# Optimization experiments

Hardware: AMD Instinct MI355X
Metric: run time of the kernel (lower is better)

Reference implementation:

```python
import jax, jax.numpy as jnp
import numpy as np
from jax import lax

H = 1024
NH = 16
R = 32
B, S = 32, 1024
LN_EPS = 1e-5

def _gelu(x):
    return jax.nn.gelu(x, approximate=False)

def setup_inputs() -> dict:
    key = jax.random.key(0)
    ks = jax.random.split(key, 24)
    w = lambda k, shape: jax.random.normal(k, shape, jnp.float32) * 0.02
    d = {}
    d['computation_results'] = jax.random.normal(ks[0], (B, S, H), jnp.float32)
    d['max_steps'] = 16
    # rule selector: Linear(H,H), GELU, Linear(H,R)
    d['rule_w1'] = w(ks[1], (H, H)); d['rule_b1'] = jnp.zeros((H,))
    d['rule_w2'] = w(ks[2], (R, H)); d['rule_b2'] = jnp.zeros((R,))
    d['rule_emb'] = jax.random.normal(ks[3], (R, H), jnp.float32)
    # MultiheadAttention packed in-proj [3H,H] and out-proj [H,H]
    d['attn_in_w'] = w(ks[4], (3 * H, H)); d['attn_in_b'] = jnp.zeros((3 * H,))
    d['attn_out_w'] = w(ks[5], (H, H)); d['attn_out_b'] = jnp.zeros((H,))
    # 2-layer LSTM, PyTorch gate order i,f,g,o
    d['lstm_wih0'] = w(ks[6], (4 * H, H)); d['lstm_whh0'] = w(ks[7], (4 * H, H))
    d['lstm_bih0'] = jnp.zeros((4 * H,)); d['lstm_bhh0'] = jnp.zeros((4 * H,))
    d['lstm_wih1'] = w(ks[8], (4 * H, H)); d['lstm_whh1'] = w(ks[9], (4 * H, H))
    d['lstm_bih1'] = jnp.zeros((4 * H,)); d['lstm_bhh1'] = jnp.zeros((4 * H,))
    # step generator: Linear(H,2H), LayerNorm(2H), GELU, Linear(2H,H)
    d['gen_w1'] = w(ks[10], (2 * H, H)); d['gen_b1'] = jnp.zeros((2 * H,))
    d['gen_ln_g'] = jnp.ones((2 * H,)); d['gen_ln_b'] = jnp.zeros((2 * H,))
    d['gen_w2'] = w(ks[11], (H, 2 * H)); d['gen_b2'] = jnp.zeros((H,))
    # step validator: Linear(2H,H), GELU, Linear(H,1), Sigmoid
    d['val_w1'] = w(ks[12], (H, 2 * H)); d['val_b1'] = jnp.zeros((H,))
    d['val_w2'] = w(ks[13], (1, H)); d['val_b2'] = jnp.zeros((1,))
    # proof verifier: Linear(H,H), GELU, Linear(H,1), Sigmoid
    d['ver_w1'] = w(ks[14], (H, H)); d['ver_b1'] = jnp.zeros((H,))
    d['ver_w2'] = w(ks[15], (1, H)); d['ver_b2'] = jnp.zeros((1,))
    return d


def reference(computation_results, max_steps, rule_w1, rule_b1, rule_w2, rule_b2, rule_emb,
              attn_in_w, attn_in_b, attn_out_w, attn_out_b,
              lstm_wih0, lstm_whh0, lstm_bih0, lstm_bhh0,
              lstm_wih1, lstm_whh1, lstm_bih1, lstm_bhh1,
              gen_w1, gen_b1, gen_ln_g, gen_ln_b, gen_w2, gen_b2,
              val_w1, val_b1, val_w2, val_b2,
              ver_w1, ver_b1, ver_w2, ver_b2):
    comp = computation_results
    b, s, h = comp.shape
    dh = h // NH
    scale = dh ** -0.5
    wq, wk, wv = jnp.split(attn_in_w, 3, axis=0)
    bq, bk, bv = jnp.split(attn_in_b, 3, axis=0)
    # K/V projections of the static context, computed once outside the step loop
    K = (comp @ wk.T + bk).reshape(b, s, NH, dh)  # [B,S,NH,dh]
    V = (comp @ wv.T + bv).reshape(b, s, NH, dh)
    lstm_params = ((lstm_wih0, lstm_whh0, lstm_bih0, lstm_bhh0),
                   (lstm_wih1, lstm_whh1, lstm_bih1, lstm_bhh1))

    def step(carry, _):
        ps, hmem, cmem = carry  # ps: [B,H]; hmem/cmem: [2,B,H]
        # rule selection
        logits = _gelu(ps @ rule_w1.T + rule_b1) @ rule_w2.T + rule_b2
        probs = jax.nn.softmax(logits, axis=-1)  # [B,R]
        sel = probs @ rule_emb  # [B,H]
        # single-query multi-head attention over computation context
        q = (ps @ wq.T + bq).reshape(b, NH, dh) * scale
        scores = jnp.einsum('bhd,bshd->bhs', q, K)
        a = jax.nn.softmax(scores, axis=-1)  # [B,NH,S]
        ctx = jnp.einsum('bhs,bshd->bhd', a, V).reshape(b, h) @ attn_out_w.T + attn_out_b
        attn_avg = a.mean(axis=1)  # head-averaged weights, [B,S]
        # 2-layer LSTM cell, one timestep
        x = ps
        hs, cs = [], []
        for l, (wih, whh, bih, bhh) in enumerate(lstm_params):
            g = x @ wih.T + bih + hmem[l] @ whh.T + bhh
            gi, gf, gg, go = jnp.split(g, 4, axis=-1)
            cn = jax.nn.sigmoid(gf) * cmem[l] + jax.nn.sigmoid(gi) * jnp.tanh(gg)
            hn = jax.nn.sigmoid(go) * jnp.tanh(cn)
            hs.append(hn); cs.append(cn); x = hn
        mem_out = x
        # step generator with LayerNorm+GELU
        si = ps + sel + ctx + mem_out
        z = si @ gen_w1.T + gen_b1
        mu = z.mean(axis=-1, keepdims=True)
        var = ((z - mu) ** 2).mean(axis=-1, keepdims=True)
        z = (z - mu) / jnp.sqrt(var + LN_EPS) * gen_ln_g + gen_ln_b
        nxt = _gelu(z) @ gen_w2.T + gen_b2
        val = jax.nn.sigmoid(_gelu(jnp.concatenate([ps, nxt], axis=-1) @ val_w1.T + val_b1) @ val_w2.T + val_b2)
        return (nxt, jnp.stack(hs), jnp.stack(cs)), (nxt, probs, val, attn_avg)

    init_state = comp[:, 0, :]
    carry0 = (init_state, jnp.zeros((2, b, h), comp.dtype), jnp.zeros((2, b, h), comp.dtype))
    (final, _, _), (steps, probs, vals, attn) = lax.scan(step, carry0, None, length=int(max_steps))
    proof_steps = jnp.concatenate([init_state[None], steps], axis=0)  # [T+1,B,H]
    proof_validity = jax.nn.sigmoid(_gelu(final @ ver_w1.T + ver_b1) @ ver_w2.T + ver_b2)  # [B,1]
    return proof_steps, proof_validity, probs, vals, attn
```

## Files before the change

kernel.cpp:

```cpp
#include <hip/hip_runtime.h>

typedef unsigned short u16;
typedef unsigned int u32;
typedef __attribute__((ext_vector_type(8))) short short8v;
typedef __attribute__((ext_vector_type(4))) float f32x4;

#define MFMA16(a,b,c) __builtin_amdgcn_mfma_f32_16x16x32_bf16((a),(b),(c),0,0,0)

__device__ __forceinline__ u16 f2bf(float f){
  u32 u = __float_as_uint(f);
  return (u16)((u + 0x7fffu + ((u >> 16) & 1u)) >> 16);
}
__device__ __forceinline__ float bf2f(u16 h){ return __uint_as_float(((u32)h) << 16); }
__device__ __forceinline__ float gelu_f(float x){ return 0.5f * x * (1.f + erff(x * 0.70710678118654752f)); }
__device__ __forceinline__ float sigm_f(float x){ return 1.f / (1.f + __expf(-x)); }
__device__ __forceinline__ void acc4(float4& a, const float4 b){ a.x+=b.x; a.y+=b.y; a.z+=b.z; a.w+=b.w; }

struct CastJobs { const float* s[13]; u16* d[13]; int start[14]; };
__global__ __launch_bounds__(256) void cast_all_k(CastJobs J){
  int bx = blockIdx.x, j = 0;
  #pragma unroll
  for (int t = 0; t < 13; t++) if (bx >= J.start[t + 1]) j = t + 1;
  int i = (bx - J.start[j]) * 1024 + threadIdx.x * 4;
  float4 v = *(const float4*)(J.s[j] + i);
  ushort4 o; o.x = f2bf(v.x); o.y = f2bf(v.y); o.z = f2bf(v.z); o.w = f2bf(v.w);
  *(ushort4*)(J.d[j] + i) = o;
}

__global__ __launch_bounds__(256) void init_k(const float* __restrict__ comp, float* ps0, float* outp,
                                              float* h0, float* c0, float* h1, float* c1){
  int i = blockIdx.x * 256 + threadIdx.x;
  int b = i >> 10, hh = i & 1023;
  float v = comp[(size_t)b * 1048576 + hh];
  ps0[i] = v; outp[i] = v;
  h0[i] = 0.f; c0[i] = 0.f; h1[i] = 0.f; c1[i] = 0.f;
}

__global__ __launch_bounds__(256) void gemmv_k(const float* __restrict__ A,
    const u16* __restrict__ W, const float* __restrict__ bias, u16* __restrict__ C)
{
  int m0 = blockIdx.x * 128, n0 = blockIdx.y * 128;
  __shared__ u16 As[128 * 32];
  __shared__ u16 Bs[128 * 32];
  int tid = threadIdx.x;
  int w = tid >> 6, l = tid & 63, lr = l & 15, lk = l >> 4;
  int wm = (w >> 1) * 64, wn = (w & 1) * 64;
  f32x4 acc[4][4];
  #pragma unroll
  for (int i = 0; i < 4; i++)
    #pragma unroll
    for (int j = 0; j < 4; j++) acc[i][j] = (f32x4){0.f,0.f,0.f,0.f};

  for (int kc = 0; kc < 1024; kc += 32){
    __syncthreads();
    #pragma unroll
    for (int u = 0; u < 4; u++){
      int i = tid + u * 256;
      int row = i >> 3, kq = (i & 7) * 4;
      float4 v = *(const float4*)(A + (size_t)(m0 + row) * 1024 + kc + kq);
      uint2 pk;
      pk.x = (u32)f2bf(v.x) | ((u32)f2bf(v.y) << 16);
      pk.y = (u32)f2bf(v.z) | ((u32)f2bf(v.w) << 16);
      *(uint2*)(As + row * 32 + kq) = pk;
    }
    #pragma unroll
    for (int u = 0; u < 2; u++){
      int i = tid + u * 256;
      int row = i >> 2, kq = (i & 3) * 8;
      *(uint4*)(Bs + row * 32 + kq) = *(const uint4*)(W + (size_t)(n0 + row) * 1024 + kc + kq);
    }
    __syncthreads();
    short8v a[4], bb[4];
    #pragma unroll
    for (int mi = 0; mi < 4; mi++) a[mi]  = *(const short8v*)(As + (wm + mi * 16 + lr) * 32 + lk * 8);
    #pragma unroll
    for (int ni = 0; ni < 4; ni++) bb[ni] = *(const short8v*)(Bs + (wn + ni * 16 + lr) * 32 + lk * 8);
    #pragma unroll
    for (int mi = 0; mi < 4; mi++)
      #pragma unroll
      for (int ni = 0; ni < 4; ni++)
        acc[mi][ni] = MFMA16(a[mi], bb[ni], acc[mi][ni]);
  }
  #pragma unroll
  for (int mi = 0; mi < 4; mi++)
    #pragma unroll
    for (int ni = 0; ni < 4; ni++)
      #pragma unroll
      for (int r = 0; r < 4; r++){
        int row = m0 + wm + mi * 16 + lk * 4 + r;
        int col = n0 + wn + ni * 16 + lr;
        C[(size_t)row * 1024 + col] = f2bf(acc[mi][ni][r] + bias[col]);
      }
}

__global__ __launch_bounds__(256) void gemmk_k(const float* __restrict__ A,
    const u16* __restrict__ W, const float* __restrict__ bias, u16* __restrict__ Kt)
{
  int n0 = blockIdx.x * 128;
  int m0 = blockIdx.y * 128;
  __shared__ u16 Ws[128 * 32];
  __shared__ u16 Cs[128 * 32];
  int tid = threadIdx.x;
  int w = tid >> 6, l = tid & 63, lr = l & 15, lk = l >> 4;
  int wm = (w >> 1) * 64, wn = (w & 1) * 64;
  f32x4 acc[4][4];
  #pragma unroll
  for (int i = 0; i < 4; i++)
    #pragma unroll
    for (int j = 0; j < 4; j++) acc[i][j] = (f32x4){0.f,0.f,0.f,0.f};

  for (int kc = 0; kc < 1024; kc += 32){
    __syncthreads();
    #pragma unroll
    for (int u = 0; u < 2; u++){
      int i = tid + u * 256;
      int row = i >> 2, kq = (i & 3) * 8;
      *(uint4*)(Ws + row * 32 + kq) = *(const uint4*)(W + (size_t)(m0 + row) * 1024 + kc + kq);
    }
    #pragma unroll
    for (int u = 0; u < 4; u++){
      int i = tid + u * 256;
      int row = i >> 3, kq = (i & 7) * 4;
      float4 v = *(const float4*)(A + (size_t)(n0 + row) * 1024 + kc + kq);
      uint2 pk;
      pk.x = (u32)f2bf(v.x) | ((u32)f2bf(v.y) << 16);
      pk.y = (u32)f2bf(v.z) | ((u32)f2bf(v.w) << 16);
      *(uint2*)(Cs + row * 32 + kq) = pk;
    }
    __syncthreads();
    short8v a[4], bb[4];
    #pragma unroll
    for (int mi = 0; mi < 4; mi++) a[mi]  = *(const short8v*)(Ws + (wm + mi * 16 + lr) * 32 + lk * 8);
    #pragma unroll
    for (int ni = 0; ni < 4; ni++) bb[ni] = *(const short8v*)(Cs + (wn + ni * 16 + lr) * 32 + lk * 8);
    #pragma unroll
    for (int mi = 0; mi < 4; mi++)
      #pragma unroll
      for (int ni = 0; ni < 4; ni++)
        acc[mi][ni] = MFMA16(a[mi], bb[ni], acc[mi][ni]);
  }
  #pragma unroll
  for (int mi = 0; mi < 4; mi++)
    #pragma unroll
    for (int ni = 0; ni < 4; ni++)
      #pragma unroll
      for (int r = 0; r < 4; r++){
        int row = m0 + wm + mi * 16 + lk * 4 + r;
        int col = n0 + wn + ni * 16 + lr;
        int b = col >> 10, s = col & 1023;
        Kt[((size_t)b * 1024 + row) * 1024 + s] = f2bf(acc[mi][ni][r] + bias[row]);
      }
}

struct LinSeg {
  const float* X0; const float* Xa; const float* Xb; const float* Xc;
  const u16* W1; const float* b1;
  const float* Y; const u16* W2; const float* b2;
  float* out; float* out2;
  int K1, ld1, K2, ld2, N, act;
  float scale;
};

__device__ __forceinline__ short8v load_sum8(const LinSeg& S, int row, int kb){
  size_t o = (size_t)row * S.K1 + kb;
  float4 v0 = *(const float4*)(S.X0 + o);
  float4 v1 = *(const float4*)(S.X0 + o + 4);
  if (S.Xa){ acc4(v0, *(const float4*)(S.Xa + o)); acc4(v1, *(const float4*)(S.Xa + o + 4)); }
  if (S.Xb){ acc4(v0, *(const float4*)(S.Xb + o)); acc4(v1, *(const float4*)(S.Xb + o + 4)); }
  if (S.Xc){ acc4(v0, *(const float4*)(S.Xc + o)); acc4(v1, *(const float4*)(S.Xc + o + 4)); }
  short8v r;
  r[0]=(short)f2bf(v0.x); r[1]=(short)f2bf(v0.y); r[2]=(short)f2bf(v0.z); r[3]=(short)f2bf(v0.w);
  r[4]=(short)f2bf(v1.x); r[5]=(short)f2bf(v1.y); r[6]=(short)f2bf(v1.z); r[7]=(short)f2bf(v1.w);
  return r;
}
__device__ __forceinline__ short8v load_y8(const float* __restrict__ p){
  float4 v0 = *(const float4*)(p);
  float4 v1 = *(const float4*)(p + 4);
  short8v r;
  r[0]=(short)f2bf(v0.x); r[1]=(short)f2bf(v0.y); r[2]=(short)f2bf(v0.z); r[3]=(short)f2bf(v0.w);
  r[4]=(short)f2bf(v1.x); r[5]=(short)f2bf(v1.y); r[6]=(short)f2bf(v1.z); r[7]=(short)f2bf(v1.w);
  return r;
}

typedef float Red32[32][32];

__device__ void lin_body(const LinSeg& S, int bi, int tid, Red32* red){
  int c0 = bi * 32;
  int w = tid >> 6, l = tid & 63, lr = l & 15, lk = l >> 4;
  f32x4 acc[2][2];
  #pragma unroll
  for (int i = 0; i < 2; i++)
    #pragma unroll
    for (int j = 0; j < 2; j++) acc[i][j] = (f32x4){0.f,0.f,0.f,0.f};

  {
    int chunk = S.K1 >> 3;
    int kb0 = w * chunk + lk * 8;
    for (int kk = 0; kk < chunk; kk += 32){
      int kb = kb0 + kk;
      short8v a0 = load_sum8(S, lr, kb);
      short8v a1 = load_sum8(S, lr + 16, kb);
      short8v w0 = *(const short8v*)(S.W1 + (size_t)(c0 + lr) * S.ld1 + kb);
      short8v w1 = *(const short8v*)(S.W1 + (size_t)(c0 + lr + 16) * S.ld1 + kb);
      acc[0][0] = MFMA16(a0, w0, acc[0][0]);
      acc[0][1] = MFMA16(a0, w1, acc[0][1]);
      acc[1][0] = MFMA16(a1, w0, acc[1][0]);
      acc[1][1] = MFMA16(a1, w1, acc[1][1]);
    }
  }
  if (S.Y){
    int chunk = S.K2 >> 3;
    int kb0 = w * chunk + lk * 8;
    for (int kk = 0; kk < chunk; kk += 32){
      int kb = kb0 + kk;
      short8v a0 = load_y8(S.Y + (size_t)lr * S.K2 + kb);
      short8v a1 = load_y8(S.Y + (size_t)(lr + 16) * S.K2 + kb);
      short8v w0 = *(const short8v*)(S.W2 + (size_t)(c0 + lr) * S.ld2 + kb);
      short8v w1 = *(const short8v*)(S.W2 + (size_t)(c0 + lr + 16) * S.ld2 + kb);
      acc[0][0] = MFMA16(a0, w0, acc[0][0]);
      acc[0][1] = MFMA16(a0, w1, acc[0][1]);
      acc[1][0] = MFMA16(a1, w0, acc[1][0]);
      acc[1][1] = MFMA16(a1, w1, acc[1][1]);
    }
  }
  #pragma unroll
  for (int mi = 0; mi < 2; mi++)
    #pragma unroll
    for (int ni = 0; ni < 2; ni++)
      #pragma unroll
      for (int r = 0; r < 4; r++)
        red[w][mi * 16 + lk * 4 + r][ni * 16 + lr] = acc[mi][ni][r];
  __syncthreads();
  for (int i = tid; i < 1024; i += 512){
    int row = i >> 5, col = i & 31;
    float v = 0.f;
    #pragma unroll
    for (int ww = 0; ww < 8; ww++) v += red[ww][row][col];
    v += S.b1[c0 + col];
    if (S.b2) v += S.b2[c0 + col];
    if (S.act == 1) v = gelu_f(v);
    else if (S.act == 2) v *= S.scale;
    S.out[(size_t)row * S.N + c0 + col] = v;
    if (S.out2) S.out2[(size_t)row * S.N + c0 + col] = v;
  }
}

__global__ __launch_bounds__(512) void linmulti_k(LinSeg s0, LinSeg s1, LinSeg s2, int n0, int n1){
  __shared__ float red[8][32][32];
  int bx = blockIdx.x, tid = threadIdx.x;
  if (bx < n0) lin_body(s0, bx, tid, red);
  else if (bx < n0 + n1) lin_body(s1, bx - n0, tid, red);
  else lin_body(s2, bx - n0 - n1, tid, red);
}

__global__ __launch_bounds__(256) void rg0_k(
    const float* __restrict__ h1a, const float* __restrict__ w2, const float* __restrict__ b2,
    const float* __restrict__ emb, float* __restrict__ probs_out, float* __restrict__ sel,
    const float* __restrict__ g, const float* __restrict__ cprev,
    float* __restrict__ cn, float* __restrict__ hn)
{
  int tid = threadIdx.x;
  if (blockIdx.x < 128){
    int idx = blockIdx.x * 256 + tid;
    int b = idx >> 10, j = idx & 1023;
    const float* gr = g + (size_t)b * 4096;
    float gi = gr[j], gf = gr[1024 + j], gg = gr[2048 + j], go = gr[3072 + j];
    float c = sigm_f(gf) * cprev[idx] + sigm_f(gi) * tanhf(gg);
    cn[idx] = c;
    hn[idx] = sigm_f(go) * tanhf(c);
    return;
  }
  int b = blockIdx.x - 128;
  __shared__ float lg[32], pshared[32];
  int j = tid >> 3, l8 = tid & 7;
  const float* xr = h1a + b * 1024;
  const float* wr = w2 + j * 1024;
  float acc = 0.f;
  #pragma unroll 8
  for (int kk = 0; kk < 32; kk++){
    int k = kk * 32 + l8 * 4;
    float4 xv = *(const float4*)(xr + k);
    float4 wv = *(const float4*)(wr + k);
    acc += xv.x * wv.x + xv.y * wv.y + xv.z * wv.z + xv.w * wv.w;
  }
  acc += __shfl_xor(acc, 1); acc += __shfl_xor(acc, 2); acc += __shfl_xor(acc, 4);
  if (l8 == 0) lg[j] = acc + b2[j];
  __syncthreads();
  if (tid < 32){
    float v = lg[tid];
    float m = v;
    for (int o = 1; o < 32; o <<= 1) m = fmaxf(m, __shfl_xor(m, o));
    float e = __expf(v - m);
    float s = e;
    for (int o = 1; o < 32; o <<= 1) s += __shfl_xor(s, o);
    float p = e / s;
    pshared[tid] = p;
    probs_out[b * 32 + tid] = p;
  }
  __syncthreads();
  for (int j2 = tid; j2 < 1024; j2 += 256){
    float a2 = 0.f;
    #pragma unroll
    for (int r = 0; r < 32; r++) a2 += pshared[r] * emb[r * 1024 + j2];
    sel[b * 1024 + j2] = a2;
  }
}

__global__ __launch_bounds__(256) void attn_k(const float* __restrict__ q,
    const u16* __restrict__ Kt, const u16* __restrict__ Vb,
    float* __restrict__ afull, float* __restrict__ ctx0)
{
  int bh = blockIdx.x;
  int b = bh >> 4, h = bh & 15;
  int tid = threadIdx.x;
  __shared__ float qs[64];
  __shared__ float sc[1024];
  __shared__ float rmx[4], rsm[4];
  __shared__ float ctxp[8][64];
  if (tid < 64) qs[tid] = q[bh * 64 + tid];
  __syncthreads();
  const u32* kt = (const u32*)(Kt + (size_t)bh * 65536);
  float a0 = 0.f, a1 = 0.f, a2 = 0.f, a3 = 0.f;
  #pragma unroll 8
  for (int d = 0; d < 64; d++){
    float qd = qs[d];
    u32 p0 = kt[d * 512 + tid];
    u32 p1 = kt[d * 512 + tid + 256];
    a0 += qd * bf2f((u16)(p0 & 0xffff)); a1 += qd * bf2f((u16)(p0 >> 16));
    a2 += qd * bf2f((u16)(p1 & 0xffff)); a3 += qd * bf2f((u16)(p1 >> 16));
  }
  float mx = fmaxf(fmaxf(a0, a1), fmaxf(a2, a3));
  for (int o = 1; o < 64; o <<= 1) mx = fmaxf(mx, __shfl_xor(mx, o));
  if ((tid & 63) == 0) rmx[tid >> 6] = mx;
  __syncthreads();
  mx = fmaxf(fmaxf(rmx[0], rmx[1]), fmaxf(rmx[2], rmx[3]));
  float e0 = __expf(a0 - mx), e1 = __expf(a1 - mx), e2 = __expf(a2 - mx), e3 = __expf(a3 - mx);
  float sm = e0 + e1 + e2 + e3;
  for (int o = 1; o < 64; o <<= 1) sm += __shfl_xor(sm, o);
  if ((tid & 63) == 0) rsm[tid >> 6] = sm;
  __syncthreads();
  sm = rsm[0] + rsm[1] + rsm[2] + rsm[3];
  float inv = 1.f / sm;
  float* ar = afull + (size_t)bh * 1024;
  float2 w0 = make_float2(e0 * inv, e1 * inv);
  float2 w1 = make_float2(e2 * inv, e3 * inv);
  *(float2*)(sc + 2 * tid) = w0;       *(float2*)(ar + 2 * tid) = w0;
  *(float2*)(sc + 512 + 2 * tid) = w1; *(float2*)(ar + 512 + 2 * tid) = w1;
  __syncthreads();
  int d2 = (tid & 31) * 2, chunk = tid >> 5;
  const u16* vb = Vb + ((size_t)(b * 1024) * 16 + h) * 64 + d2;
  float c0 = 0.f, c1 = 0.f;
  for (int s = chunk * 128; s < chunk * 128 + 128; s++){
    u32 vv = *(const u32*)(vb + (size_t)s * 1024);
    float wv = sc[s];
    c0 += wv * bf2f((u16)(vv & 0xffff));
    c1 += wv * bf2f((u16)(vv >> 16));
  }
  *(float2*)&ctxp[chunk][d2] = make_float2(c0, c1);
  __syncthreads();
  if (tid < 64){
    float r = 0.f;
    #pragma unroll
    for (int c = 0; c < 8; c++) r += ctxp[c][tid];
    ctx0[bh * 64 + tid] = r;
  }
}

__global__ __launch_bounds__(256) void ga1_k(const float* __restrict__ g, const float* __restrict__ cprev,
                                             float* __restrict__ cn, float* __restrict__ hn,
                                             const float* __restrict__ afull, float* __restrict__ aout){
  int idx = blockIdx.x * 256 + threadIdx.x;
  int b = idx >> 10, j = idx & 1023;
  const float* gr = g + (size_t)b * 4096;
  float gi = gr[j], gf = gr[1024 + j], gg = gr[2048 + j], go = gr[3072 + j];
  float c = sigm_f(gf) * cprev[idx] + sigm_f(gi) * tanhf(gg);
  cn[idx] = c;
  hn[idx] = sigm_f(go) * tanhf(c);
  float acc = 0.f;
  #pragma unroll
  for (int hh = 0; hh < 16; hh++) acc += afull[((size_t)(b * 16 + hh)) * 1024 + j];
  aout[idx] = acc * (1.f / 16.f);
}

__global__ __launch_bounds__(256) void lngelu_k(const float* __restrict__ z, const float* __restrict__ g,
                                                const float* __restrict__ bta, float* __restrict__ zg){
  int bb = blockIdx.x, tid = threadIdx.x;
  const float* zr = z + (size_t)bb * 2048;
  float v[8]; float s = 0.f;
  #pragma unroll
  for (int i = 0; i < 8; i++){ v[i] = zr[tid + i * 256]; s += v[i]; }
  __shared__ float red[4], red2[4];
  for (int o = 1; o < 64; o <<= 1) s += __shfl_xor(s, o);
  if ((tid & 63) == 0) red[tid >> 6] = s;
  __syncthreads();
  float mu = (red[0] + red[1] + red[2] + red[3]) * (1.f / 2048.f);
  float s2 = 0.f;
  #pragma unroll
  for (int i = 0; i < 8; i++){ float d = v[i] - mu; s2 += d * d; }
  for (int o = 1; o < 64; o <<= 1) s2 += __shfl_xor(s2, o);
  if ((tid & 63) == 0) red2[tid >> 6] = s2;
  __syncthreads();
  float var = (red2[0] + red2[1] + red2[2] + red2[3]) * (1.f / 2048.f);
  float rstd = rsqrtf(var + 1e-5f);
  float* zo = zg + (size_t)bb * 2048;
  #pragma unroll
  for (int i = 0; i < 8; i++){
    int idx = tid + i * 256;
    float y = (v[i] - mu) * rstd * g[idx] + bta[idx];
    zo[idx] = gelu_f(y);
  }
}

__global__ __launch_bounds__(256) void dotsig_k(const float* __restrict__ x, const float* __restrict__ w,
                                                const float* __restrict__ bias, float* __restrict__ out){
  int b = threadIdx.x >> 3, l8 = threadIdx.x & 7;
  const float* xr = x + (size_t)b * 1024;
  float acc = 0.f;
  #pragma unroll 8
  for (int kk = 0; kk < 32; kk++){
    int k = kk * 32 + l8 * 4;
    float4 xv = *(const float4*)(xr + k);
    float4 wv = *(const float4*)(w + k);
    acc += xv.x * wv.x + xv.y * wv.y + xv.z * wv.z + xv.w * wv.w;
  }
  acc += __shfl_xor(acc, 1); acc += __shfl_xor(acc, 2); acc += __shfl_xor(acc, 4);
  if (l8 == 0) out[b] = sigm_f(acc + bias[0]);
}

extern "C" void kernel_launch(void* const* d_in, const int* in_sizes, int n_in,
                              void* d_out, int out_size, void* d_ws, size_t ws_size,
                              hipStream_t stream) {
  const float* comp      = (const float*)d_in[0];
  const float* rule_w1   = (const float*)d_in[2];
  const float* rule_b1   = (const float*)d_in[3];
  const float* rule_w2   = (const float*)d_in[4];
  const float* rule_b2   = (const float*)d_in[5];
  const float* rule_emb  = (const float*)d_in[6];
  const float* attn_in_w = (const float*)d_in[7];
  const float* attn_in_b = (const float*)d_in[8];
  const float* attn_out_w= (const float*)d_in[9];
  const float* attn_out_b= (const float*)d_in[10];
  const float* wih0 = (const float*)d_in[11];
  const float* whh0 = (const float*)d_in[12];
  const float* bih0 = (const float*)d_in[13];
  const float* bhh0 = (const float*)d_in[14];
  const float* wih1 = (const float*)d_in[15];
  const float* whh1 = (const float*)d_in[16];
  const float* bih1 = (const float*)d_in[17];
  const float* bhh1 = (const float*)d_in[18];
  const float* gen_w1 = (const float*)d_in[19];
  const float* gen_b1 = (const float*)d_in[20];
  const float* ln_g   = (const float*)d_in[21];
  const float* ln_b   = (const float*)d_in[22];
  const float* gen_w2 = (const float*)d_in[23];
  const float* gen_b2 = (const float*)d_in[24];
  const float* val_w1 = (const float*)d_in[25];
  const float* val_b1 = (const float*)d_in[26];
  const float* val_w2 = (const float*)d_in[27];
  const float* val_b2 = (const float*)d_in[28];
  const float* ver_w1 = (const float*)d_in[29];
  const float* ver_b1 = (const float*)d_in[30];
  const float* ver_w2 = (const float*)d_in[31];
  const float* ver_b2 = (const float*)d_in[32];

  float* out_f     = (float*)d_out;
  float* out_proof = out_f;
  float* out_valid = out_f + 17 * 32768;
  float* out_probs = out_valid + 32;
  float* out_vals  = out_probs + 16 * 1024;
  float* out_attn  = out_vals + 16 * 32;

  char* wp = (char*)d_ws;
  auto carve = [&](size_t bytes) -> void* {
    void* p = (void*)wp; wp += (bytes + 255) & ~(size_t)255; return p;
  };
  u16* Kt    = (u16*)carve((size_t)33554432 * 2);
  u16* Vb    = (u16*)carve((size_t)33554432 * 2);
  u16* rw1b  = (u16*)carve(2097152);
  u16* wqb   = (u16*)carve(2097152);
  u16* wkb   = (u16*)carve(2097152);
  u16* wvb   = (u16*)carve(2097152);
  u16* aowb  = (u16*)carve(2097152);
  u16* wih0b = (u16*)carve(8388608);
  u16* whh0b = (u16*)carve(8388608);
  u16* wih1b = (u16*)carve(8388608);
  u16* whh1b = (u16*)carve(8388608);
  u16* gw1b  = (u16*)carve(4194304);
  u16* gw2b  = (u16*)carve(4194304);
  u16* vw1b  = (u16*)carve(4194304);
  u16* verw1b= (u16*)carve(2097152);
  float* psb[2]  = { (float*)carve(131072), (float*)carve(131072) };
  float* h0b[2]  = { (float*)carve(131072), (float*)carve(131072) };
  float* c0b[2]  = { (float*)carve(131072), (float*)carve(131072) };
  float* h1b[2]  = { (float*)carve(131072), (float*)carve(131072) };
  float* c1b[2]  = { (float*)carve(131072), (float*)carve(131072) };
  float* h1act = (float*)carve(131072);
  float* sel   = (float*)carve(131072);
  float* qbuf  = (float*)carve(131072);
  float* ctx0  = (float*)carve(131072);
  float* ctxb  = (float*)carve(131072);
  float* v1buf = (float*)carve(131072);
  float* gbuf  = (float*)carve(524288);
  float* zbuf  = (float*)carve(262144);
  float* zgbuf = (float*)carve(262144);
  float* afull = (float*)carve(2097152);
  (void)ws_size; (void)in_sizes; (void)n_in; (void)out_size;

  CastJobs J;
  const float* srcs[13] = { rule_w1, attn_in_w, attn_in_w + 1048576, attn_in_w + 2097152,
                            attn_out_w, wih0, whh0, wih1, whh1, gen_w1, gen_w2, val_w1, ver_w1 };
  u16* dsts[13] = { rw1b, wqb, wkb, wvb, aowb, wih0b, whh0b, wih1b, whh1b, gw1b, gw2b, vw1b, verw1b };
  int sizes[13] = { 1048576, 1048576, 1048576, 1048576, 1048576,
                    4194304, 4194304, 4194304, 4194304, 2097152, 2097152, 2097152, 1048576 };
  int st = 0;
  for (int i = 0; i < 13; i++){ J.s[i] = srcs[i]; J.d[i] = dsts[i]; J.start[i] = st; st += sizes[i] / 1024; }
  J.start[13] = st;
  cast_all_k<<<dim3(st), dim3(256), 0, stream>>>(J);

  gemmk_k<<<dim3(256, 8), dim3(256), 0, stream>>>(comp, wkb, attn_in_b + 1024, Kt);
  gemmv_k<<<dim3(256, 8), dim3(256), 0, stream>>>(comp, wvb, attn_in_b + 2048, Vb);

  init_k<<<dim3(128), dim3(256), 0, stream>>>(comp, psb[0], out_proof,
      h0b[0], c0b[0], h1b[0], c1b[0]);

  auto mkseg = [&](const float* X0, const float* Xa, const float* Xb, const float* Xc,
                   int K1, const u16* W1, int ld1, const float* bb1,
                   const float* Y, int K2, const u16* W2, int ld2, const float* bb2,
                   float* out, int N, int act, float scl, float* out2) -> LinSeg {
    LinSeg S; S.X0 = X0; S.Xa = Xa; S.Xb = Xb; S.Xc = Xc; S.K1 = K1; S.W1 = W1; S.ld1 = ld1; S.b1 = bb1;
    S.Y = Y; S.K2 = K2; S.W2 = W2; S.ld2 = ld2; S.b2 = bb2;
    S.out = out; S.N = N; S.act = act; S.scale = scl; S.out2 = out2;
    return S;
  };
  auto lin1 = [&](LinSeg S){
    linmulti_k<<<dim3(S.N / 32), dim3(512), 0, stream>>>(S, S, S, S.N / 32, 0);
  };

  for (int t = 0; t < 16; t++){
    int cur = t & 1, nx = cur ^ 1;
    float* ps = psb[cur];
    LinSeg sRule = mkseg(ps, 0, 0, 0, 1024, rw1b, 1024, rule_b1, 0, 0, 0, 0, 0, h1act, 1024, 1, 0.f, 0);
    LinSeg sQ    = mkseg(ps, 0, 0, 0, 1024, wqb, 1024, attn_in_b, 0, 0, 0, 0, 0, qbuf, 1024, 2, 0.125f, 0);
    LinSeg sL0   = mkseg(ps, 0, 0, 0, 1024, wih0b, 1024, bih0, h0b[cur], 1024, whh0b, 1024, bhh0,
                         gbuf, 4096, 0, 0.f, 0);
    linmulti_k<<<dim3(192), dim3(512), 0, stream>>>(sRule, sQ, sL0, 32, 32);
    attn_k<<<dim3(512), dim3(256), 0, stream>>>(qbuf, Kt, Vb, afull, ctx0);
    rg0_k<<<dim3(160), dim3(256), 0, stream>>>(h1act, rule_w2, rule_b2, rule_emb,
        out_probs + t * 1024, sel, gbuf, c0b[cur], c0b[nx], h0b[nx]);
    LinSeg sCtx = mkseg(ctx0, 0, 0, 0, 1024, aowb, 1024, attn_out_b, 0, 0, 0, 0, 0, ctxb, 1024, 0, 0.f, 0);
    LinSeg sL1  = mkseg(h0b[nx], 0, 0, 0, 1024, wih1b, 1024, bih1, h1b[cur], 1024, whh1b, 1024, bhh1,
                        gbuf, 4096, 0, 0.f, 0);
    linmulti_k<<<dim3(160), dim3(512), 0, stream>>>(sCtx, sL1, sL1, 32, 128);
    ga1_k<<<dim3(128), dim3(256), 0, stream>>>(gbuf, c1b[cur], c1b[nx], h1b[nx],
        afull, out_attn + (size_t)t * 32768);
    LinSeg sG1 = mkseg(ps, sel, ctxb, h1b[nx], 1024, gw1b, 1024, gen_b1, 0, 0, 0, 0, 0,
                       zbuf, 2048, 0, 0.f, 0);
    lin1(sG1);
    lngelu_k<<<dim3(32), dim3(256), 0, stream>>>(zbuf, ln_g, ln_b, zgbuf);
    LinSeg sG2 = mkseg(zgbuf, 0, 0, 0, 2048, gw2b, 2048, gen_b2, 0, 0, 0, 0, 0,
                       psb[nx], 1024, 0, 0.f, out_proof + (size_t)(t + 1) * 32768);
    lin1(sG2);
    LinSeg sV = mkseg(ps, 0, 0, 0, 1024, vw1b, 2048, val_b1, psb[nx], 1024, vw1b + 1024, 2048, 0,
                      v1buf, 1024, 1, 0.f, 0);
    lin1(sV);
    dotsig_k<<<dim3(1), dim3(256), 0, stream>>>(v1buf, val_w2, val_b2, out_vals + t * 32);
  }
  LinSeg sVer = mkseg(psb[0], 0, 0, 0, 1024, verw1b, 1024, ver_b1, 0, 0, 0, 0, 0,
                      v1buf, 1024, 1, 0.f, 0);
  lin1(sVer);
  dotsig_k<<<dim3(1), dim3(256), 0, stream>>>(v1buf, ver_w2, ver_b2, out_valid);
}
```

Measured before the change: 2.220 ms.

## Fuse K/V projections, LN-GELU into GEMM, and batch validator work out of loop

The input is pre-cast to bf16 once, and the K and V projections run in one merged kernel that stages tiles with direct global-to-LDS loads. The per-step LayerNorm kernel is removed. Row statistics are accumulated atomically in the first generator GEMM's epilogue, and normalisation plus GELU are applied while loading operands for the second GEMM. The attention kernel is merged with the rule-selection and LSTM layer-0 kernel. The per-step validator, verifier and attention-average work is deferred and batched into single launches after the loop, reusing the compb buffer to hold all attention maps. Together these cut launches and serial per-step work, at the cost of a single-pass variance formula and atomics.

```diff
diff --git a/kernel.cpp b/kernel.cpp
--- a/kernel.cpp
+++ b/kernel.cpp
@@ -15,6 +15,11 @@
 __device__ __forceinline__ float gelu_f(float x){ return 0.5f * x * (1.f + erff(x * 0.70710678118654752f)); }
 __device__ __forceinline__ float sigm_f(float x){ return 1.f / (1.f + __expf(-x)); }
 __device__ __forceinline__ void acc4(float4& a, const float4 b){ a.x+=b.x; a.y+=b.y; a.z+=b.z; a.w+=b.w; }
+
+__device__ __forceinline__ void gl16(const void* g, void* l){
+  __builtin_amdgcn_global_load_lds((const __attribute__((address_space(1))) u32*)g,
+                                   (__attribute__((address_space(3))) u32*)l, 16, 0, 0);
+}
 
 struct CastJobs { const float* s[13]; u16* d[13]; int start[14]; };
 __global__ __launch_bounds__(256) void cast_all_k(CastJobs J){
@@ -27,6 +32,15 @@
   *(ushort4*)(J.d[j] + i) = o;
 }
 
+__global__ __launch_bounds__(256) void cast_k(const float* __restrict__ s, u16* __restrict__ d, int n){
+  int i = (blockIdx.x * 256 + threadIdx.x) * 4;
+  if (i + 3 < n){
+    float4 v = *(const float4*)(s + i);
+    ushort4 o; o.x = f2bf(v.x); o.y = f2bf(v.y); o.z = f2bf(v.z); o.w = f2bf(v.w);
+    *(ushort4*)(d + i) = o;
+  }
+}
+
 __global__ __launch_bounds__(256) void init_k(const float* __restrict__ comp, float* ps0, float* outp,
                                               float* h0, float* c0, float* h1, float* c1){
   int i = blockIdx.x * 256 + threadIdx.x;
@@ -36,13 +50,19 @@
   h0[i] = 0.f; c0[i] = 0.f; h1[i] = 0.f; c1[i] = 0.f;
 }
 
-__global__ __launch_bounds__(256) void gemmv_k(const float* __restrict__ A,
-    const u16* __restrict__ W, const float* __restrict__ bias, u16* __restrict__ C)
+__global__ __launch_bounds__(256) void gemmkv_k(const u16* __restrict__ compb,
+    const u16* __restrict__ Wk, const u16* __restrict__ Wv,
+    const float* __restrict__ bk, const float* __restrict__ bv,
+    u16* __restrict__ Kt, u16* __restrict__ Vb)
 {
-  int m0 = blockIdx.x * 128, n0 = blockIdx.y * 128;
   __shared__ u16 As[128 * 32];
   __shared__ u16 Bs[128 * 32];
   int tid = threadIdx.x;
+  const u16 *msrc, *nsrc;
+  int m0, n0, isK = (blockIdx.z != 0);
+  if (!isK){ m0 = blockIdx.x * 128; n0 = blockIdx.y * 128; msrc = compb; nsrc = Wv; }
+  else     { m0 = blockIdx.y * 128; n0 = blockIdx.x * 128; msrc = Wk;    nsrc = compb; }
+
   int w = tid >> 6, l = tid & 63, lr = l & 15, lk = l >> 4;
   int wm = (w >> 1) * 64, wn = (w & 1) * 64;
   f32x4 acc[4][4];
@@ -51,23 +71,14 @@
     #pragma unroll
     for (int j = 0; j < 4; j++) acc[i][j] = (f32x4){0.f,0.f,0.f,0.f};
 
+  int row0 = tid >> 2, k80 = (tid & 3) * 8;
   for (int kc = 0; kc < 1024; kc += 32){
-    __syncthreads();
-    #pragma unroll
-    for (int u = 0; u < 4; u++){
-      int i = tid + u * 256;
-      int row = i >> 3, kq = (i & 7) * 4;
-      float4 v = *(const float4*)(A + (size_t)(m0 + row) * 1024 + kc + kq);
-      uint2 pk;
-      pk.x = (u32)f2bf(v.x) | ((u32)f2bf(v.y) << 16);
-      pk.y = (u32)f2bf(v.z) | ((u32)f2bf(v.w) << 16);
-      *(uint2*)(As + row * 32 + kq) = pk;
-    }
-    #pragma unroll
-    for (int u = 0; u < 2; u++){
-      int i = tid + u * 256;
-      int row = i >> 2, kq = (i & 3) * 8;
-      *(uint4*)(Bs + row * 32 + kq) = *(const uint4*)(W + (size_t)(n0 + row) * 1024 + kc + kq);
+    #pragma unroll
+    for (int r = 0; r < 2; r++){
+      int i = tid + r * 256;
+      int row = row0 + r * 64, k8 = k80;
+      gl16(msrc + (size_t)(m0 + row) * 1024 + kc + k8, As + i * 8);
+      gl16(nsrc + (size_t)(n0 + row) * 1024 + kc + k8, Bs + i * 8);
     }
     __syncthreads();
     short8v a[4], bb[4];
@@ -80,6 +91,7 @@
       #pragma unroll
       for (int ni = 0; ni < 4; ni++)
         acc[mi][ni] = MFMA16(a[mi], bb[ni], acc[mi][ni]);
+    __syncthreads();
   }
   #pragma unroll
   for (int mi = 0; mi < 4; mi++)
@@ -89,66 +101,12 @@
       for (int r = 0; r < 4; r++){
         int row = m0 + wm + mi * 16 + lk * 4 + r;
         int col = n0 + wn + ni * 16 + lr;
-        C[(size_t)row * 1024 + col] = f2bf(acc[mi][ni][r] + bias[col]);
-      }
-}
-
-__global__ __launch_bounds__(256) void gemmk_k(const float* __restrict__ A,
-    const u16* __restrict__ W, const float* __restrict__ bias, u16* __restrict__ Kt)
-{
-  int n0 = blockIdx.x * 128;
-  int m0 = blockIdx.y * 128;
-  __shared__ u16 Ws[128 * 32];
-  __shared__ u16 Cs[128 * 32];
-  int tid = threadIdx.x;
-  int w = tid >> 6, l = tid & 63, lr = l & 15, lk = l >> 4;
-  int wm = (w >> 1) * 64, wn = (w & 1) * 64;
-  f32x4 acc[4][4];
-  #pragma unroll
-  for (int i = 0; i < 4; i++)
-    #pragma unroll
-    for (int j = 0; j < 4; j++) acc[i][j] = (f32x4){0.f,0.f,0.f,0.f};
-
-  for (int kc = 0; kc < 1024; kc += 32){
-    __syncthreads();
-    #pragma unroll
-    for (int u = 0; u < 2; u++){
-      int i = tid + u * 256;
-      int row = i >> 2, kq = (i & 3) * 8;
-      *(uint4*)(Ws + row * 32 + kq) = *(const uint4*)(W + (size_t)(m0 + row) * 1024 + kc + kq);
-    }
-    #pragma unroll
-    for (int u = 0; u < 4; u++){
-      int i = tid + u * 256;
-      int row = i >> 3, kq = (i & 7) * 4;
-      float4 v = *(const float4*)(A + (size_t)(n0 + row) * 1024 + kc + kq);
-      uint2 pk;
-      pk.x = (u32)f2bf(v.x) | ((u32)f2bf(v.y) << 16);
-      pk.y = (u32)f2bf(v.z) | ((u32)f2bf(v.w) << 16);
-      *(uint2*)(Cs + row * 32 + kq) = pk;
-    }
-    __syncthreads();
-    short8v a[4], bb[4];
-    #pragma unroll
-    for (int mi = 0; mi < 4; mi++) a[mi]  = *(const short8v*)(Ws + (wm + mi * 16 + lr) * 32 + lk * 8);
-    #pragma unroll
-    for (int ni = 0; ni < 4; ni++) bb[ni] = *(const short8v*)(Cs + (wn + ni * 16 + lr) * 32 + lk * 8);
-    #pragma unroll
-    for (int mi = 0; mi < 4; mi++)
-      #pragma unroll
-      for (int ni = 0; ni < 4; ni++)
-        acc[mi][ni] = MFMA16(a[mi], bb[ni], acc[mi][ni]);
-  }
-  #pragma unroll
-  for (int mi = 0; mi < 4; mi++)
-    #pragma unroll
-    for (int ni = 0; ni < 4; ni++)
-      #pragma unroll
-      for (int r = 0; r < 4; r++){
-        int row = m0 + wm + mi * 16 + lk * 4 + r;
-        int col = n0 + wn + ni * 16 + lr;
-        int b = col >> 10, s = col & 1023;
-        Kt[((size_t)b * 1024 + row) * 1024 + s] = f2bf(acc[mi][ni][r] + bias[row]);
+        if (!isK){
+          Vb[(size_t)row * 1024 + col] = f2bf(acc[mi][ni][r] + bv[col]);
+        } else {
+          int b = col >> 10, s = col & 1023;
+          Kt[((size_t)b * 1024 + row) * 1024 + s] = f2bf(acc[mi][ni][r] + bk[row]);
+        }
       }
 }
 
@@ -159,27 +117,44 @@
   float* out; float* out2;
   int K1, ld1, K2, ld2, N, act;
   float scale;
+  float* stats;
+  const float* lng; const float* lnb; const float* lnstats;
 };
+
+__device__ __forceinline__ short8v pack8(float4 v0, float4 v1){
+  short8v r;
+  r[0]=(short)f2bf(v0.x); r[1]=(short)f2bf(v0.y); r[2]=(short)f2bf(v0.z); r[3]=(short)f2bf(v0.w);
+  r[4]=(short)f2bf(v1.x); r[5]=(short)f2bf(v1.y); r[6]=(short)f2bf(v1.z); r[7]=(short)f2bf(v1.w);
+  return r;
+}
 
 __device__ __forceinline__ short8v load_sum8(const LinSeg& S, int row, int kb){
   size_t o = (size_t)row * S.K1 + kb;
   float4 v0 = *(const float4*)(S.X0 + o);
   float4 v1 = *(const float4*)(S.X0 + o + 4);
-  if (S.Xa){ acc4(v0, *(const float4*)(S.Xa + o)); acc4(v1, *(const float4*)(S.Xa + o + 4)); }
-  if (S.Xb){ acc4(v0, *(const float4*)(S.Xb + o)); acc4(v1, *(const float4*)(S.Xb + o + 4)); }
-  if (S.Xc){ acc4(v0, *(const float4*)(S.Xc + o)); acc4(v1, *(const float4*)(S.Xc + o + 4)); }
-  short8v r;
-  r[0]=(short)f2bf(v0.x); r[1]=(short)f2bf(v0.y); r[2]=(short)f2bf(v0.z); r[3]=(short)f2bf(v0.w);
-  r[4]=(short)f2bf(v1.x); r[5]=(short)f2bf(v1.y); r[6]=(short)f2bf(v1.z); r[7]=(short)f2bf(v1.w);
-  return r;
+  if (S.lng){
+    float mu = S.lnstats[row] * (1.f / 2048.f);
+    float ms = S.lnstats[32 + row] * (1.f / 2048.f);
+    float rstd = rsqrtf(ms - mu * mu + 1e-5f);
+    float4 g0 = *(const float4*)(S.lng + kb), g1 = *(const float4*)(S.lng + kb + 4);
+    float4 b0 = *(const float4*)(S.lnb + kb), b1 = *(const float4*)(S.lnb + kb + 4);
+    v0.x = gelu_f((v0.x - mu) * rstd * g0.x + b0.x);
+    v0.y = gelu_f((v0.y - mu) * rstd * g0.y + b0.y);
+    v0.z = gelu_f((v0.z - mu) * rstd * g0.z + b0.z);
+    v0.w = gelu_f((v0.w - mu) * rstd * g0.w + b0.w);
+    v1.x = gelu_f((v1.x - mu) * rstd * g1.x + b1.x);
+    v1.y = gelu_f((v1.y - mu) * rstd * g1.y + b1.y);
+    v1.z = gelu_f((v1.z - mu) * rstd * g1.z + b1.z);
+    v1.w = gelu_f((v1.w - mu) * rstd * g1.w + b1.w);
+  } else {
+    if (S.Xa){ acc4(v0, *(const float4*)(S.Xa + o)); acc4(v1, *(const float4*)(S.Xa + o + 4)); }
+    if (S.Xb){ acc4(v0, *(const float4*)(S.Xb + o)); acc4(v1, *(const float4*)(S.Xb + o + 4)); }
+    if (S.Xc){ acc4(v0, *(const float4*)(S.Xc + o)); acc4(v1, *(const float4*)(S.Xc + o + 4)); }
+  }
+  return pack8(v0, v1);
 }
 __device__ __forceinline__ short8v load_y8(const float* __restrict__ p){
-  float4 v0 = *(const float4*)(p);
-  float4 v1 = *(const float4*)(p + 4);
-  short8v r;
-  r[0]=(short)f2bf(v0.x); r[1]=(short)f2bf(v0.y); r[2]=(short)f2bf(v0.z); r[3]=(short)f2bf(v0.w);
-  r[4]=(short)f2bf(v1.x); r[5]=(short)f2bf(v1.y); r[6]=(short)f2bf(v1.z); r[7]=(short)f2bf(v1.w);
-  return r;
+  return pack8(*(const float4*)(p), *(const float4*)(p + 4));
 }
 
 typedef float Red32[32][32];
@@ -231,6 +206,8 @@
       for (int r = 0; r < 4; r++)
         red[w][mi * 16 + lk * 4 + r][ni * 16 + lr] = acc[mi][ni][r];
   __syncthreads();
+  float vout[2]; int iout[2];
+  int cnt = 0;
   for (int i = tid; i < 1024; i += 512){
     int row = i >> 5, col = i & 31;
     float v = 0.f;
@@ -242,6 +219,21 @@
     else if (S.act == 2) v *= S.scale;
     S.out[(size_t)row * S.N + c0 + col] = v;
     if (S.out2) S.out2[(size_t)row * S.N + c0 + col] = v;
+    vout[cnt] = v; iout[cnt] = i; cnt++;
+  }
+  if (S.stats){
+    __syncthreads();
+    float* rf = (float*)red;
+    rf[iout[0]] = vout[0]; rf[1024 + iout[0]] = vout[0] * vout[0];
+    rf[iout[1]] = vout[1]; rf[1024 + iout[1]] = vout[1] * vout[1];
+    __syncthreads();
+    if (tid < 32){
+      float s = 0.f, s2 = 0.f;
+      #pragma unroll
+      for (int cc = 0; cc < 32; cc++){ s += rf[tid * 32 + cc]; s2 += rf[1024 + tid * 32 + cc]; }
+      atomicAdd(S.stats + tid, s);
+      atomicAdd(S.stats + 32 + tid, s2);
+    }
   }
 }
 
@@ -253,15 +245,58 @@
   else lin_body(s2, bx - n0 - n1, tid, red);
 }
 
-__global__ __launch_bounds__(256) void rg0_k(
+__global__ __launch_bounds__(512) void valver_k(const u16* __restrict__ vw1, const float* __restrict__ vb1,
+    const u16* __restrict__ verw1, const float* __restrict__ verb1,
+    const float* __restrict__ proof, float* __restrict__ v1){
+  __shared__ float red[8][32][32];
+  int t = blockIdx.y;
+  LinSeg S = {};
+  if (t < 16){
+    S.X0 = proof + (size_t)t * 32768; S.K1 = 1024; S.W1 = vw1; S.ld1 = 2048; S.b1 = vb1;
+    S.Y = proof + (size_t)(t + 1) * 32768; S.K2 = 1024; S.W2 = vw1 + 1024; S.ld2 = 2048;
+  } else {
+    S.X0 = proof + (size_t)16 * 32768; S.K1 = 1024; S.W1 = verw1; S.ld1 = 1024; S.b1 = verb1;
+  }
+  S.out = v1 + (size_t)t * 32768; S.N = 1024; S.act = 1;
+  lin_body(S, blockIdx.x, threadIdx.x, red);
+}
+
+__global__ __launch_bounds__(256) void dotsig_b_k(const float* __restrict__ v1,
+    const float* __restrict__ w2v, const float* __restrict__ b2v,
+    const float* __restrict__ w2ver, const float* __restrict__ b2ver,
+    float* __restrict__ out_vals, float* __restrict__ out_valid){
+  int t = blockIdx.x;
+  const float* w = (t < 16) ? w2v : w2ver;
+  const float* bs = (t < 16) ? b2v : b2ver;
+  const float* x = v1 + (size_t)t * 32768;
+  int b = threadIdx.x >> 3, l8 = threadIdx.x & 7;
+  const float* xr = x + (size_t)b * 1024;
+  float acc = 0.f;
+  #pragma unroll 8
+  for (int kk = 0; kk < 32; kk++){
+    int k = kk * 32 + l8 * 4;
+    float4 xv = *(const float4*)(xr + k);
+    float4 wv = *(const float4*)(w + k);
+    acc += xv.x * wv.x + xv.y * wv.y + xv.z * wv.z + xv.w * wv.w;
+  }
+  acc += __shfl_xor(acc, 1); acc += __shfl_xor(acc, 2); acc += __shfl_xor(acc, 4);
+  if (l8 == 0){
+    float r = sigm_f(acc + bs[0]);
+    if (t < 16) out_vals[t * 32 + b] = r; else out_valid[b] = r;
+  }
+}
+
+__global__ __launch_bounds__(256) void attn_rg0_k(const float* __restrict__ q,
+    const u16* __restrict__ Kt, const u16* __restrict__ Vb,
+    float* __restrict__ afull, float* __restrict__ ctx0,
     const float* __restrict__ h1a, const float* __restrict__ w2, const float* __restrict__ b2,
     const float* __restrict__ emb, float* __restrict__ probs_out, float* __restrict__ sel,
     const float* __restrict__ g, const float* __restrict__ cprev,
     float* __restrict__ cn, float* __restrict__ hn)
 {
   int tid = threadIdx.x;
-  if (blockIdx.x < 128){
-    int idx = blockIdx.x * 256 + tid;
+  if (blockIdx.x >= 544){
+    int idx = (blockIdx.x - 544) * 256 + tid;
     int b = idx >> 10, j = idx & 1023;
     const float* gr = g + (size_t)b * 4096;
     float gi = gr[j], gf = gr[1024 + j], gg = gr[2048 + j], go = gr[3072 + j];
@@ -270,49 +305,45 @@
     hn[idx] = sigm_f(go) * tanhf(c);
     return;
   }
-  int b = blockIdx.x - 128;
-  __shared__ float lg[32], pshared[32];
-  int j = tid >> 3, l8 = tid & 7;
-  const float* xr = h1a + b * 1024;
-  const float* wr = w2 + j * 1024;
-  float acc = 0.f;
-  #pragma unroll 8
-  for (int kk = 0; kk < 32; kk++){
-    int k = kk * 32 + l8 * 4;
-    float4 xv = *(const float4*)(xr + k);
-    float4 wv = *(const float4*)(wr + k);
-    acc += xv.x * wv.x + xv.y * wv.y + xv.z * wv.z + xv.w * wv.w;
-  }
-  acc += __shfl_xor(acc, 1); acc += __shfl_xor(acc, 2); acc += __shfl_xor(acc, 4);
-  if (l8 == 0) lg[j] = acc + b2[j];
-  __syncthreads();
-  if (tid < 32){
-    float v = lg[tid];
-    float m = v;
-    for (int o = 1; o < 32; o <<= 1) m = fmaxf(m, __shfl_xor(m, o));
-    float e = __expf(v - m);
-    float s = e;
-    for (int o = 1; o < 32; o <<= 1) s += __shfl_xor(s, o);
-    float p = e / s;
-    pshared[tid] = p;
-    probs_out[b * 32 + tid] = p;
-  }
-  __syncthreads();
-  for (int j2 = tid; j2 < 1024; j2 += 256){
-    float a2 = 0.f;
-    #pragma unroll
-    for (int r = 0; r < 32; r++) a2 += pshared[r] * emb[r * 1024 + j2];
-    sel[b * 1024 + j2] = a2;
-  }
-}
-
-__global__ __launch_bounds__(256) void attn_k(const float* __restrict__ q,
-    const u16* __restrict__ Kt, const u16* __restrict__ Vb,
-    float* __restrict__ afull, float* __restrict__ ctx0)
-{
+  if (blockIdx.x >= 512){
+    int b = blockIdx.x - 512;
+    __shared__ float lg[32], pshared[32];
+    int j = tid >> 3, l8 = tid & 7;
+    const float* xr = h1a + b * 1024;
+    const float* wr = w2 + j * 1024;
+    float acc = 0.f;
+    #pragma unroll 8
+    for (int kk = 0; kk < 32; kk++){
+      int k = kk * 32 + l8 * 4;
+      float4 xv = *(const float4*)(xr + k);
+      float4 wv = *(const float4*)(wr + k);
+      acc += xv.x * wv.x + xv.y * wv.y + xv.z * wv.z + xv.w * wv.w;
+    }
+    acc += __shfl_xor(acc, 1); acc += __shfl_xor(acc, 2); acc += __shfl_xor(acc, 4);
+    if (l8 == 0) lg[j] = acc + b2[j];
+    __syncthreads();
+    if (tid < 32){
+      float v = lg[tid];
+      float m = v;
+      for (int o = 1; o < 32; o <<= 1) m = fmaxf(m, __shfl_xor(m, o));
+      float e = __expf(v - m);
+      float s = e;
+      for (int o = 1; o < 32; o <<= 1) s += __shfl_xor(s, o);
+      float p = e / s;
+      pshared[tid] = p;
+      probs_out[b * 32 + tid] = p;
+    }
+    __syncthreads();
+    for (int j2 = tid; j2 < 1024; j2 += 256){
+      float a2 = 0.f;
+      #pragma unroll
+      for (int r = 0; r < 32; r++) a2 += pshared[r] * emb[r * 1024 + j2];
+      sel[b * 1024 + j2] = a2;
+    }
+    return;
+  }
   int bh = blockIdx.x;
   int b = bh >> 4, h = bh & 15;
-  int tid = threadIdx.x;
   __shared__ float qs[64];
   __shared__ float sc[1024];
   __shared__ float rmx[4], rsm[4];
@@ -366,9 +397,10 @@
   }
 }
 
-__global__ __launch_bounds__(256) void ga1_k(const float* __restrict__ g, const float* __restrict__ cprev,
-                                             float* __restrict__ cn, float* __restrict__ hn,
-                                             const float* __restrict__ afull, float* __restrict__ aout){
+__global__ __launch_bounds__(256) void gz_k(const float* __restrict__ g, const float* __restrict__ cprev,
+                                            float* __restrict__ cn, float* __restrict__ hn,
+                                            float* __restrict__ stats){
+  if (blockIdx.x == 0 && threadIdx.x < 64) stats[threadIdx.x] = 0.f;
   int idx = blockIdx.x * 256 + threadIdx.x;
   int b = idx >> 10, j = idx & 1023;
   const float* gr = g + (size_t)b * 4096;
@@ -376,55 +408,17 @@
   float c = sigm_f(gf) * cprev[idx] + sigm_f(gi) * tanhf(gg);
   cn[idx] = c;
   hn[idx] = sigm_f(go) * tanhf(c);
+}
+
+__global__ __launch_bounds__(256) void attnavg_all_k(const float* __restrict__ afull, float* __restrict__ out){
+  int idx = blockIdx.x * 256 + threadIdx.x;
+  int t = idx >> 15, r = idx & 32767;
+  int b = r >> 10, s = r & 1023;
+  const float* base = afull + (size_t)t * 524288 + (size_t)b * 16384;
   float acc = 0.f;
   #pragma unroll
-  for (int hh = 0; hh < 16; hh++) acc += afull[((size_t)(b * 16 + hh)) * 1024 + j];
-  aout[idx] = acc * (1.f / 16.f);
-}
-
-__global__ __launch_bounds__(256) void lngelu_k(const float* __restrict__ z, const float* __restrict__ g,
-                                                const float* __restrict__ bta, float* __restrict__ zg){
-  int bb = blockIdx.x, tid = threadIdx.x;
-  const float* zr = z + (size_t)bb * 2048;
-  float v[8]; float s = 0.f;
-  #pragma unroll
-  for (int i = 0; i < 8; i++){ v[i] = zr[tid + i * 256]; s += v[i]; }
-  __shared__ float red[4], red2[4];
-  for (int o = 1; o < 64; o <<= 1) s += __shfl_xor(s, o);
-  if ((tid & 63) == 0) red[tid >> 6] = s;
-  __syncthreads();
-  float mu = (red[0] + red[1] + red[2] + red[3]) * (1.f / 2048.f);
-  float s2 = 0.f;
-  #pragma unroll
-  for (int i = 0; i < 8; i++){ float d = v[i] - mu; s2 += d * d; }
-  for (int o = 1; o < 64; o <<= 1) s2 += __shfl_xor(s2, o);
-  if ((tid & 63) == 0) red2[tid >> 6] = s2;
-  __syncthreads();
-  float var = (red2[0] + red2[1] + red2[2] + red2[3]) * (1.f / 2048.f);
-  float rstd = rsqrtf(var + 1e-5f);
-  float* zo = zg + (size_t)bb * 2048;
-  #pragma unroll
-  for (int i = 0; i < 8; i++){
-    int idx = tid + i * 256;
-    float y = (v[i] - mu) * rstd * g[idx] + bta[idx];
-    zo[idx] = gelu_f(y);
-  }
-}
-
-__global__ __launch_bounds__(256) void dotsig_k(const float* __restrict__ x, const float* __restrict__ w,
-                                                const float* __restrict__ bias, float* __restrict__ out){
-  int b = threadIdx.x >> 3, l8 = threadIdx.x & 7;
-  const float* xr = x + (size_t)b * 1024;
-  float acc = 0.f;
-  #pragma unroll 8
-  for (int kk = 0; kk < 32; kk++){
-    int k = kk * 32 + l8 * 4;
-    float4 xv = *(const float4*)(xr + k);
-    float4 wv = *(const float4*)(w + k);
-    acc += xv.x * wv.x + xv.y * wv.y + xv.z * wv.z + xv.w * wv.w;
-  }
-  acc += __shfl_xor(acc, 1); acc += __shfl_xor(acc, 2); acc += __shfl_xor(acc, 4);
-  if (l8 == 0) out[b] = sigm_f(acc + bias[0]);
+  for (int h = 0; h < 16; h++) acc += base[h * 1024 + s];
+  out[idx] = acc * (1.f / 16.f);
 }
 
 extern "C" void kernel_launch(void* const* d_in, const int* in_sizes, int n_in,
@@ -476,6 +470,8 @@
   };
   u16* Kt    = (u16*)carve((size_t)33554432 * 2);
   u16* Vb    = (u16*)carve((size_t)33554432 * 2);
+  u16* compb = (u16*)carve((size_t)33554432 * 2);
+  float* afull_all = (float*)compb;
   u16* rw1b  = (u16*)carve(2097152);
   u16* wqb   = (u16*)carve(2097152);
   u16* wkb   = (u16*)carve(2097152);
@@ -499,11 +495,10 @@
   float* qbuf  = (float*)carve(131072);
   float* ctx0  = (float*)carve(131072);
   float* ctxb  = (float*)carve(131072);
-  float* v1buf = (float*)carve(131072);
   float* gbuf  = (float*)carve(524288);
   float* zbuf  = (float*)carve(262144);
-  float* zgbuf = (float*)carve(262144);
-  float* afull = (float*)carve(2097152);
+  float* v1buf = (float*)carve(2228224);
+  float* lnstats = (float*)carve(256);
   (void)ws_size; (void)in_sizes; (void)n_in; (void)out_size;
 
   CastJobs J;
@@ -516,9 +511,10 @@
   for (int i = 0; i < 13; i++){ J.s[i] = srcs[i]; J.d[i] = dsts[i]; J.start[i] = st; st += sizes[i] / 1024; }
   J.start[13] = st;
   cast_all_k<<<dim3(st), dim3(256), 0, stream>>>(J);
-
-  gemmk_k<<<dim3(256, 8), dim3(256), 0, stream>>>(comp, wkb, attn_in_b + 1024, Kt);
-  gemmv_k<<<dim3(256, 8), dim3(256), 0, stream>>>(comp, wvb, attn_in_b + 2048, Vb);
+  cast_k<<<dim3(32768), dim3(256), 0, stream>>>(comp, compb, 33554432);
+
+  gemmkv_k<<<dim3(256, 8, 2), dim3(256), 0, stream>>>(compb, wkb, wvb,
+      attn_in_b + 1024, attn_in_b + 2048, Kt, Vb);
 
   init_k<<<dim3(128), dim3(256), 0, stream>>>(comp, psb[0], out_proof,
       h0b[0], c0b[0], h1b[0], c1b[0]);
@@ -527,7 +523,8 @@
                    int K1, const u16* W1, int ld1, const float* bb1,
                    const float* Y, int K2, const u16* W2, int ld2, const float* bb2,
                    float* out, int N, int act, float scl, float* out2) -> LinSeg {
-    LinSeg S; S.X0 = X0; S.Xa = Xa; S.Xb = Xb; S.Xc = Xc; S.K1 = K1; S.W1 = W1; S.ld1 = ld1; S.b1 = bb1;
+    LinSeg S = {};
+    S.X0 = X0; S.Xa = Xa; S.Xb = Xb; S.Xc = Xc; S.K1 = K1; S.W1 = W1; S.ld1 = ld1; S.b1 = bb1;
     S.Y = Y; S.K2 = K2; S.W2 = W2; S.ld2 = ld2; S.b2 = bb2;
     S.out = out; S.N = N; S.act = act; S.scale = scl; S.out2 = out2;
     return S;
@@ -539,34 +536,31 @@
   for (int t = 0; t < 16; t++){
     int cur = t & 1, nx = cur ^ 1;
     float* ps = psb[cur];
+    float* afull_t = afull_all + (size_t)t * 524288;
     LinSeg sRule = mkseg(ps, 0, 0, 0, 1024, rw1b, 1024, rule_b1, 0, 0, 0, 0, 0, h1act, 1024, 1, 0.f, 0);
     LinSeg sQ    = mkseg(ps, 0, 0, 0, 1024, wqb, 1024, attn_in_b, 0, 0, 0, 0, 0, qbuf, 1024, 2, 0.125f, 0);
     LinSeg sL0   = mkseg(ps, 0, 0, 0, 1024, wih0b, 1024, bih0, h0b[cur], 1024, whh0b, 1024, bhh0,
                          gbuf, 4096, 0, 0.f, 0);
     linmulti_k<<<dim3(192), dim3(512), 0, stream>>>(sRule, sQ, sL0, 32, 32);
-    attn_k<<<dim3(512), dim3(256), 0, stream>>>(qbuf, Kt, Vb, afull, ctx0);
-    rg0_k<<<dim3(160), dim3(256), 0, stream>>>(h1act, rule_w2, rule_b2, rule_emb,
-        out_probs + t * 1024, sel, gbuf, c0b[cur], c0b[nx], h0b[nx]);
+    attn_rg0_k<<<dim3(672), dim3(256), 0, stream>>>(qbuf, Kt, Vb, afull_t, ctx0,
+        h1act, rule_w2, rule_b2, rule_emb, out_probs + t * 1024, sel,
+        gbuf, c0b[cur], c0b[nx], h0b[nx]);
     LinSeg sCtx = mkseg(ctx0, 0, 0, 0, 1024, aowb, 1024, attn_out_b, 0, 0, 0, 0, 0, ctxb, 1024, 0, 0.f, 0);
     LinSeg sL1  = mkseg(h0b[nx], 0, 0, 0, 1024, wih1b, 1024, bih1, h1b[cur], 1024, whh1b, 1024, bhh1,
                         gbuf, 4096, 0, 0.f, 0);
     linmulti_k<<<dim3(160), dim3(512), 0, stream>>>(sCtx, sL1, sL1, 32, 128);
-    ga1_k<<<dim3(128), dim3(256), 0, stream>>>(gbuf, c1b[cur], c1b[nx], h1b[nx],
-        afull, out_attn + (size_t)t * 32768);
+    gz_k<<<dim3(128), dim3(256), 0, stream>>>(gbuf, c1b[cur], c1b[nx], h1b[nx], lnstats);
     LinSeg sG1 = mkseg(ps, sel, ctxb, h1b[nx], 1024, gw1b, 1024, gen_b1, 0, 0, 0, 0, 0,
                        zbuf, 2048, 0, 0.f, 0);
+    sG1.stats = lnstats;
     lin1(sG1);
-    lngelu_k<<<dim3(32), dim3(256), 0, stream>>>(zbuf, ln_g, ln_b, zgbuf);
-    LinSeg sG2 = mkseg(zgbuf, 0, 0, 0, 2048, gw2b, 2048, gen_b2, 0, 0, 0, 0, 0,
+    LinSeg sG2 = mkseg(zbuf, 0, 0, 0, 2048, gw2b, 2048, gen_b2, 0, 0, 0, 0, 0,
                        psb[nx], 1024, 0, 0.f, out_proof + (size_t)(t + 1) * 32768);
+    sG2.lng = ln_g; sG2.lnb = ln_b; sG2.lnstats = lnstats;
     lin1(sG2);
-    LinSeg sV = mkseg(ps, 0, 0, 0, 1024, vw1b, 2048, val_b1, psb[nx], 1024, vw1b + 1024, 2048, 0,
-                      v1buf, 1024, 1, 0.f, 0);
-    lin1(sV);
-    dotsig_k<<<dim3(1), dim3(256), 0, stream>>>(v1buf, val_w2, val_b2, out_vals + t * 32);
-  }
-  LinSeg sVer = mkseg(psb[0], 0, 0, 0, 1024, verw1b, 1024, ver_b1, 0, 0, 0, 0, 0,
-                      v1buf, 1024, 1, 0.f, 0);
-  lin1(sVer);
-  dotsig_k<<<dim3(1), dim3(256), 0, stream>>>(v1buf, ver_w2, ver_b2, out_valid);
-}
+  }
+  valver_k<<<dim3(32, 17), dim3(512), 0, stream>>>(vw1b, val_b1, verw1b, ver_b1, out_proof, v1buf);
+  dotsig_b_k<<<dim3(17), dim3(256), 0, stream>>>(v1buf, val_w2, val_b2, ver_w2, ver_b2,
+      out_vals, out_valid);
+  attnavg_all_k<<<dim3(2048), dim3(256), 0, stream>>>(afull_all, out_attn);
+}
```

After: 1.948 ms. 12.2% less time.
